# Performance work log

Measured on AMD Instinct MI355X. Metric: run time of the kernel, lower is better.

Reference implementation:

```python
import jax, jax.numpy as jnp
import numpy as np

N_NODES = 100000
N_EDGES = 1600000
D = 128


def setup_inputs() -> dict:
    key = jax.random.key(0)
    k1, k2, k3 = jax.random.split(key, 3)
    x = jax.random.normal(k1, (N_NODES, D), dtype=jnp.float32)
    edge_index = jax.random.randint(k2, (2, N_EDGES), 0, N_NODES, dtype=jnp.int64)
    weight = jax.random.normal(k3, (D, D), dtype=jnp.float32) * (1.0 / np.sqrt(D))
    bias = jnp.zeros((D,), dtype=jnp.float32)
    return {"x": x, "edge_index": edge_index, "weight": weight, "bias": bias}


def reference(x, edge_index, weight, bias):
    # Eval-mode forward: dropout(p=0.5, training=False) is identity.
    N = x.shape[0]
    row, col = edge_index[0], edge_index[1]  # source -> target

    # gcn_norm: add self loops (weight 1), symmetric normalization
    loop = jnp.arange(N, dtype=edge_index.dtype)
    full_row = jnp.concatenate([row, loop])
    full_col = jnp.concatenate([col, loop])
    ew = jnp.ones(full_row.shape[0], dtype=x.dtype)
    deg = jax.ops.segment_sum(ew, full_col, num_segments=N)
    deg_inv_sqrt = jnp.where(deg > 0, jax.lax.rsqrt(jnp.maximum(deg, 1e-12)), 0.0)
    norm = deg_inv_sqrt[full_row] * ew * deg_inv_sqrt[full_col]  # [E+N]

    # linear transform then gather-scale-scatter aggregation
    h = x @ weight.T  # [N, D]
    msgs = h[full_row] * norm[:, None]  # [E+N, D]
    out = jax.ops.segment_sum(msgs, full_col, num_segments=N)
    out = out + bias
    return jax.nn.relu(out)
```

## Files before the change

kernel.cpp:

```cpp
#include <hip/hip_runtime.h>

#define N_NODES 100000
#define N_EDGES 1600000
#define D 128
#define N_STRIPS (N_NODES / 32)

#define BSH   9
#define NBKT  196
#define P_BLK 512
#define EPB   (N_EDGES / P_BLK)
#define ARENA 9216

typedef __bf16 bf16x4 __attribute__((ext_vector_type(4)));
typedef __bf16 bf16x8 __attribute__((ext_vector_type(8)));
typedef float  f32x4  __attribute__((ext_vector_type(4)));

__device__ __forceinline__ void acc8(float (&a)[8], uint4 v) {
    a[0] += __uint_as_float(v.x << 16);
    a[1] += __uint_as_float(v.x & 0xFFFF0000u);
    a[2] += __uint_as_float(v.y << 16);
    a[3] += __uint_as_float(v.y & 0xFFFF0000u);
    a[4] += __uint_as_float(v.z << 16);
    a[5] += __uint_as_float(v.z & 0xFFFF0000u);
    a[6] += __uint_as_float(v.w << 16);
    a[7] += __uint_as_float(v.w & 0xFFFF0000u);
}

__device__ __forceinline__ void gather_node(const int* __restrict__ srcs,
                                            int s, int n,
                                            const unsigned char* hbase,
                                            size_t boff, int lane, int q,
                                            float (&acc)[8]) {
    for (int base = 0; base < n; base += 64) {
        int m = n - base; if (m > 64) m = 64;
        int src_l = (lane < m) ? srcs[s + base + lane] : 0;
        int i = 0;
        for (; i + 4 <= m; i += 4) {
            int sj = __shfl(src_l, i + q);
            uint4 v = *(const uint4*)(hbase + ((size_t)sj + boff));
            acc8(acc, v);
        }
        if (i < m) {
            int sj = __shfl(src_l, i + q);
            if (q < m - i) {
                uint4 v = *(const uint4*)(hbase + ((size_t)sj + boff));
                acc8(acc, v);
            }
        }
    }
}

__global__ __launch_bounds__(1024) void k_scatter(const int* __restrict__ row,
                                                  const int* __restrict__ col,
                                                  const float4* __restrict__ w4,
                                                  int* __restrict__ gcnt,
                                                  unsigned* __restrict__ grec,
                                                  bf16x4* __restrict__ wb4) {
    int b = blockIdx.x, t = threadIdx.x;
    if (b == P_BLK) {
        for (int i = t; i < (D * D) / 4; i += 1024) {
            float4 u = w4[i];
            bf16x4 p;
            p[0] = (__bf16)u.x; p[1] = (__bf16)u.y;
            p[2] = (__bf16)u.z; p[3] = (__bf16)u.w;
            wb4[i] = p;
        }
        return;
    }
    __shared__ int      rec[EPB];
    __shared__ unsigned short kb[EPB];
    __shared__ int      srt[EPB];
    __shared__ int      dofp[EPB];
    __shared__ int      lh[256];
    __shared__ int      sc[256];
    __shared__ int      cur[256];
    __shared__ int      dofk[256];
    if (t < 256) lh[t] = 0;
    __syncthreads();
    int e0 = b * EPB;
    for (int i = t; i < EPB; i += 1024) {
        int r = row[e0 + i], c = col[e0 + i];
        int k = c >> BSH;
        rec[i] = (r << BSH) | (c & ((1 << BSH) - 1));
        kb[i]  = (unsigned short)k;
        atomicAdd(&lh[k], 1);
    }
    __syncthreads();
    int v = 0;
    if (t < 256) { v = lh[t]; sc[t] = v; }
    __syncthreads();
    for (int off = 1; off < 256; off <<= 1) {
        int u = 0;
        if (t < 256 && t >= off) u = sc[t - off];
        __syncthreads();
        if (t < 256) sc[t] += u;
        __syncthreads();
    }
    if (t < 256) {
        int excl = sc[t] - v;
        sc[t]  = excl;
        cur[t] = 0;
        int base = (t < NBKT && v > 0) ? atomicAdd(&gcnt[t], v) : 0;
        dofk[t] = t * ARENA + base - excl;
    }
    __syncthreads();
    for (int i = t; i < EPB; i += 1024) {
        int k = kb[i];
        int p = sc[k] + atomicAdd(&cur[k], 1);
        srt[p]  = rec[i];
        dofp[p] = dofk[k];
    }
    __syncthreads();
    for (int i = t; i < EPB; i += 1024) {
        unsigned dst = (unsigned)(i + dofp[i]);
        if (dst < (unsigned)(NBKT * ARENA))
            grec[dst] = (unsigned)srt[i];
    }
}

__global__ __launch_bounds__(1024) void k_fine(unsigned* __restrict__ grec,
                                               const int* __restrict__ gcnt,
                                               int* __restrict__ deg,
                                               float* __restrict__ dis,
                                               int* __restrict__ start) {
    __shared__ unsigned cache[ARENA];
    __shared__ int fh[512];
    __shared__ int fsc[512];
    int b = blockIdx.x;
    int tid = threadIdx.x;
    int cnt = gcnt[b]; if (cnt > ARENA) cnt = ARENA;
    int gs = b * ARENA;
    if (tid < 512) fh[tid] = 0;
    __syncthreads();
    for (int i = tid; i < cnt; i += 1024) {
        unsigned r = grec[gs + i];
        cache[i] = r;
        atomicAdd(&fh[r & 511], 1);
    }
    __syncthreads();
    int v = 0;
    if (tid < 512) { v = fh[tid]; fsc[tid] = v; }
    __syncthreads();
    for (int off = 1; off < 512; off <<= 1) {
        int u = 0;
        if (tid < 512 && tid >= off) u = fsc[tid - off];
        __syncthreads();
        if (tid < 512) fsc[tid] += u;
        __syncthreads();
    }
    if (tid < 512) {
        int excl = fsc[tid] - v;
        int node = (b << BSH) + tid;
        if (node < N_NODES) {
            deg[node]   = v;
            dis[node]   = rsqrtf((float)v + 1.0f);
            start[node] = gs + excl;
        }
        fh[tid] = excl;
    }
    __syncthreads();
    for (int i = tid; i < cnt; i += 1024) {
        unsigned r = cache[i];
        int pos = atomicAdd(&fh[r & 511], 1);
        grec[gs + pos] = (r >> BSH) << 8;
    }
}

__global__ __launch_bounds__(256) void k_hx(const float* __restrict__ x,
                                            const __bf16* __restrict__ wb,
                                            const float* __restrict__ dis,
                                            __bf16* __restrict__ hb) {
    int wave = threadIdx.x >> 6;
    int lane = threadIdx.x & 63;
    int strip = blockIdx.x * 4 + wave;
    if (strip >= N_STRIPS) return;
    int m0 = strip * 32;
    int l15 = lane & 15;
    int kq  = lane >> 4;

    bf16x8 a[2][4];
    #pragma unroll
    for (int mt = 0; mt < 2; ++mt) {
        const float* ap = x + (size_t)(m0 + mt * 16 + l15) * D + kq * 8;
        #pragma unroll
        for (int ks = 0; ks < 4; ++ks) {
            float4 lo = *(const float4*)(ap + ks * 32);
            float4 hi = *(const float4*)(ap + ks * 32 + 4);
            bf16x8 t;
            t[0] = (__bf16)lo.x; t[1] = (__bf16)lo.y;
            t[2] = (__bf16)lo.z; t[3] = (__bf16)lo.w;
            t[4] = (__bf16)hi.x; t[5] = (__bf16)hi.y;
            t[6] = (__bf16)hi.z; t[7] = (__bf16)hi.w;
            a[mt][ks] = t;
        }
    }

    f32x4 acc[2][8] = {};
    #pragma unroll
    for (int ks = 0; ks < 4; ++ks) {
        #pragma unroll
        for (int nt = 0; nt < 8; ++nt) {
            bf16x8 b = *(const bf16x8*)(wb + (size_t)(nt * 16 + l15) * D + ks * 32 + kq * 8);
            acc[0][nt] = __builtin_amdgcn_mfma_f32_16x16x32_bf16(a[0][ks], b, acc[0][nt], 0, 0, 0);
            acc[1][nt] = __builtin_amdgcn_mfma_f32_16x16x32_bf16(a[1][ks], b, acc[1][nt], 0, 0, 0);
        }
    }

    float dsv[2][4];
    #pragma unroll
    for (int mt = 0; mt < 2; ++mt)
        #pragma unroll
        for (int r = 0; r < 4; ++r)
            dsv[mt][r] = dis[m0 + mt * 16 + kq * 4 + r];

    #pragma unroll
    for (int nt = 0; nt < 8; ++nt) {
        int colj = nt * 16 + l15;
        #pragma unroll
        for (int mt = 0; mt < 2; ++mt) {
            #pragma unroll
            for (int r = 0; r < 4; ++r) {
                int rowi = m0 + mt * 16 + kq * 4 + r;
                hb[(size_t)rowi * D + colj] = (__bf16)(acc[mt][nt][r] * dsv[mt][r]);
            }
        }
    }
}

__global__ __launch_bounds__(256) void k_aggregate(const int* __restrict__ srcs,
                                                   const int* __restrict__ start,
                                                   const int* __restrict__ deg,
                                                   const __bf16* __restrict__ hb,
                                                   const float* __restrict__ dis,
                                                   const float* __restrict__ bias,
                                                   float* __restrict__ out) {
    int wid = (blockIdx.x * 256 + threadIdx.x) >> 6;
    int nodeA = wid * 2;
    if (nodeA >= N_NODES) return;
    int nodeB = nodeA + 1;
    int lane = threadIdx.x & 63;
    int li = lane & 15;
    int q  = lane >> 4;
    const unsigned char* hbase = (const unsigned char*)hb;
    size_t boff = (size_t)li * 16;

    int sA = start[nodeA], nA = deg[nodeA];
    int sB = start[nodeB], nB = deg[nodeB];
    float dA = dis[nodeA], dB = dis[nodeB];

    uint4 selfA = *(const uint4*)(hbase + ((size_t)nodeA * 256 + boff));
    uint4 selfB = *(const uint4*)(hbase + ((size_t)nodeB * 256 + boff));

    float accA[8] = {0.f, 0.f, 0.f, 0.f, 0.f, 0.f, 0.f, 0.f};
    float accB[8] = {0.f, 0.f, 0.f, 0.f, 0.f, 0.f, 0.f, 0.f};

    if (nA <= 64 && nB <= 64) {
        int srcA = (lane < nA) ? srcs[sA + lane] : 0;
        int srcB = (lane < nB) ? srcs[sB + lane] : 0;
        int nmax = nA > nB ? nA : nB;
        #pragma unroll
        for (int i = 0; i < 64; i += 16) {
            if (i >= nmax) break;
            int svA[4], svB[4];
            #pragma unroll
            for (int j = 0; j < 4; ++j) {
                svA[j] = __shfl(srcA, i + 4 * j + q);
                svB[j] = __shfl(srcB, i + 4 * j + q);
            }
            uint4 avA[4], avB[4];
            if (i < nA) {
                #pragma unroll
                for (int j = 0; j < 4; ++j)
                    avA[j] = *(const uint4*)(hbase + ((size_t)svA[j] + boff));
            }
            if (i < nB) {
                #pragma unroll
                for (int j = 0; j < 4; ++j)
                    avB[j] = *(const uint4*)(hbase + ((size_t)svB[j] + boff));
            }
            if (i < nA) {
                #pragma unroll
                for (int j = 0; j < 4; ++j)
                    if (i + 4 * j + q < nA) acc8(accA, avA[j]);
            }
            if (i < nB) {
                #pragma unroll
                for (int j = 0; j < 4; ++j)
                    if (i + 4 * j + q < nB) acc8(accB, avB[j]);
            }
        }
    } else {
        gather_node(srcs, sA, nA, hbase, boff, lane, q, accA);
        gather_node(srcs, sB, nB, hbase, boff, lane, q, accB);
    }

    #pragma unroll
    for (int k = 0; k < 8; ++k) {
        accA[k] += __shfl_xor(accA[k], 16);
        accA[k] += __shfl_xor(accA[k], 32);
        accB[k] += __shfl_xor(accB[k], 16);
        accB[k] += __shfl_xor(accB[k], 32);
    }

    if (q == 0) {
        acc8(accA, selfA);
        acc8(accB, selfB);

        float4 b0 = *(const float4*)(bias + li * 8);
        float4 b1 = *(const float4*)(bias + li * 8 + 4);
        float4 r0, r1;
        r0.x = fmaxf(accA[0] * dA + b0.x, 0.f);
        r0.y = fmaxf(accA[1] * dA + b0.y, 0.f);
        r0.z = fmaxf(accA[2] * dA + b0.z, 0.f);
        r0.w = fmaxf(accA[3] * dA + b0.w, 0.f);
        r1.x = fmaxf(accA[4] * dA + b1.x, 0.f);
        r1.y = fmaxf(accA[5] * dA + b1.y, 0.f);
        r1.z = fmaxf(accA[6] * dA + b1.z, 0.f);
        r1.w = fmaxf(accA[7] * dA + b1.w, 0.f);
        *(float4*)(out + (size_t)nodeA * D + li * 8)     = r0;
        *(float4*)(out + (size_t)nodeA * D + li * 8 + 4) = r1;

        r0.x = fmaxf(accB[0] * dB + b0.x, 0.f);
        r0.y = fmaxf(accB[1] * dB + b0.y, 0.f);
        r0.z = fmaxf(accB[2] * dB + b0.z, 0.f);
        r0.w = fmaxf(accB[3] * dB + b0.w, 0.f);
        r1.x = fmaxf(accB[4] * dB + b1.x, 0.f);
        r1.y = fmaxf(accB[5] * dB + b1.y, 0.f);
        r1.z = fmaxf(accB[6] * dB + b1.z, 0.f);
        r1.w = fmaxf(accB[7] * dB + b1.w, 0.f);
        *(float4*)(out + (size_t)nodeB * D + li * 8)     = r0;
        *(float4*)(out + (size_t)nodeB * D + li * 8 + 4) = r1;
    }
}

extern "C" void kernel_launch(void* const* d_in, const int* in_sizes, int n_in,
                              void* d_out, int out_size, void* d_ws, size_t ws_size,
                              hipStream_t stream) {
    const float* x    = (const float*)d_in[0];
    const int*   ei   = (const int*)d_in[1];
    const float* w    = (const float*)d_in[2];
    const float* bias = (const float*)d_in[3];
    float* out = (float*)d_out;

    char* ws = (char*)d_ws;
    int*      deg    = (int*)ws;              ws += N_NODES * 4;
    float*    dis    = (float*)ws;            ws += N_NODES * 4;
    int*      start  = (int*)ws;              ws += N_NODES * 4;
    int*      gcnt   = (int*)ws;              ws += 256 * 4;
    __bf16*   wb     = (__bf16*)ws;           ws += D * D * 2;
    unsigned* arena  = (unsigned*)ws;         ws += (size_t)NBKT * ARENA * 4;
    __bf16*   hb     = (__bf16*)ws;

    const int* row = ei;
    const int* col = ei + N_EDGES;

    hipMemsetAsync(gcnt, 0, 256 * 4, stream);
    k_scatter  <<<P_BLK + 1, 1024, 0, stream>>>(row, col, (const float4*)w, gcnt, arena, (bf16x4*)wb);
    k_fine     <<<NBKT, 1024, 0, stream>>>(arena, gcnt, deg, dis, start);
    k_hx       <<<(N_STRIPS + 3) / 4, 256, 0, stream>>>(x, wb, dis, hb);
    k_aggregate<<<(N_NODES / 2 * 64) / 256, 256, 0, stream>>>((const int*)arena, start, deg, hb, dis, bias, out);
}
```

Baseline: 222.7 us.

## Fuse coarse scatter and fine bucket sort into one kernel with grid barrier

Merges the coarse partition kernel and the per-bucket fine sort into a single persistent kernel. A global atomic counter acts as a grid-wide barrier, and the shared-memory arena is reused between the two phases. Partition blocks are halved to 256 so that all blocks can be co-resident and the barrier cannot deadlock, with the weight bf16 conversion moved to block NBKT after the barrier. This removes one kernel launch and its drain gap, at the cost of a spin barrier, fewer and larger partition blocks, and a reliance on every block being resident at once.

```diff
diff --git a/kernel.cpp b/kernel.cpp
--- a/kernel.cpp
+++ b/kernel.cpp
@@ -7,7 +7,7 @@
 
 #define BSH   9
 #define NBKT  196
-#define P_BLK 512
+#define P_BLK 256
 #define EPB   (N_EDGES / P_BLK)
 #define ARENA 9216
 
@@ -50,14 +50,121 @@
     }
 }
 
-__global__ __launch_bounds__(1024) void k_scatter(const int* __restrict__ row,
-                                                  const int* __restrict__ col,
-                                                  const float4* __restrict__ w4,
-                                                  int* __restrict__ gcnt,
-                                                  unsigned* __restrict__ grec,
-                                                  bf16x4* __restrict__ wb4) {
+__global__ __launch_bounds__(1024) void k_part(const int* __restrict__ row,
+                                               const int* __restrict__ col,
+                                               const float4* __restrict__ w4,
+                                               int* __restrict__ gcnt,
+                                               unsigned* __restrict__ arena,
+                                               bf16x4* __restrict__ wb4,
+                                               int* __restrict__ deg,
+                                               float* __restrict__ dis,
+                                               int* __restrict__ start) {
+    __shared__ unsigned smem[23040];
     int b = blockIdx.x, t = threadIdx.x;
-    if (b == P_BLK) {
+    int* done = gcnt + 256;
+
+    {
+        int*            rec  = (int*)smem;
+        unsigned short* kb   = (unsigned short*)(smem + 6272);
+        int*            srt  = (int*)(smem + 9408);
+        int*            dofp = (int*)(smem + 15680);
+        int*            lh   = (int*)(smem + 21952);
+        int*            sc   = lh + 256;
+        int*            cur  = sc + 256;
+        int*            dofk = cur + 256;
+
+        if (t < 256) lh[t] = 0;
+        __syncthreads();
+        int e0 = b * EPB;
+        for (int i = t; i < EPB; i += 1024) {
+            int r = row[e0 + i], c = col[e0 + i];
+            int k = c >> BSH;
+            rec[i] = (r << BSH) | (c & ((1 << BSH) - 1));
+            kb[i]  = (unsigned short)k;
+            atomicAdd(&lh[k], 1);
+        }
+        __syncthreads();
+        int v = 0;
+        if (t < 256) { v = lh[t]; sc[t] = v; }
+        __syncthreads();
+        for (int off = 1; off < 256; off <<= 1) {
+            int u = 0;
+            if (t < 256 && t >= off) u = sc[t - off];
+            __syncthreads();
+            if (t < 256) sc[t] += u;
+            __syncthreads();
+        }
+        if (t < 256) {
+            int excl = sc[t] - v;
+            sc[t]  = excl;
+            cur[t] = 0;
+            int base = (t < NBKT && v > 0) ? atomicAdd(&gcnt[t], v) : 0;
+            dofk[t] = t * ARENA + base - excl;
+        }
+        __syncthreads();
+        for (int i = t; i < EPB; i += 1024) {
+            int k = kb[i];
+            int p = sc[k] + atomicAdd(&cur[k], 1);
+            srt[p]  = rec[i];
+            dofp[p] = dofk[k];
+        }
+        __syncthreads();
+        for (int i = t; i < EPB; i += 1024) {
+            unsigned dst = (unsigned)(i + dofp[i]);
+            if (dst < (unsigned)(NBKT * ARENA))
+                arena[dst] = (unsigned)srt[i];
+        }
+    }
+
+    __syncthreads();
+    if (t == 0) {
+        __threadfence();
+        __hip_atomic_fetch_add(done, 1, __ATOMIC_ACQ_REL, __HIP_MEMORY_SCOPE_AGENT);
+        while (__hip_atomic_load(done, __ATOMIC_ACQUIRE, __HIP_MEMORY_SCOPE_AGENT) < P_BLK) {}
+    }
+    __syncthreads();
+
+    if (b < NBKT) {
+        unsigned* cache = smem;
+        int*      fh    = (int*)(smem + 9216);
+        int*      fsc   = (int*)(smem + 9728);
+        int cnt = gcnt[b]; if (cnt > ARENA) cnt = ARENA;
+        int gs = b * ARENA;
+        if (t < 512) fh[t] = 0;
+        __syncthreads();
+        for (int i = t; i < cnt; i += 1024) {
+            unsigned r = arena[gs + i];
+            cache[i] = r;
+            atomicAdd(&fh[r & 511], 1);
+        }
+        __syncthreads();
+        int v = 0;
+        if (t < 512) { v = fh[t]; fsc[t] = v; }
+        __syncthreads();
+        for (int off = 1; off < 512; off <<= 1) {
+            int u = 0;
+            if (t < 512 && t >= off) u = fsc[t - off];
+            __syncthreads();
+            if (t < 512) fsc[t] += u;
+            __syncthreads();
+        }
+        if (t < 512) {
+            int excl = fsc[t] - v;
+            int node = (b << BSH) + t;
+            if (node < N_NODES) {
+                deg[node]   = v;
+                dis[node]   = rsqrtf((float)v + 1.0f);
+                start[node] = gs + excl;
+            }
+            fh[t] = excl;
+        }
+        __syncthreads();
+        for (int i = t; i < cnt; i += 1024) {
+            unsigned r = cache[i];
+            int pos = atomicAdd(&fh[r & 511], 1);
+            arena[gs + pos] = (r >> BSH) << 8;
+        }
+    } else if (b == NBKT) {
         for (int i = t; i < (D * D) / 4; i += 1024) {
             float4 u = w4[i];
             bf16x4 p;
@@ -65,104 +172,6 @@
             p[2] = (__bf16)u.z; p[3] = (__bf16)u.w;
             wb4[i] = p;
         }
-        return;
-    }
-    __shared__ int      rec[EPB];
-    __shared__ unsigned short kb[EPB];
-    __shared__ int      srt[EPB];
-    __shared__ int      dofp[EPB];
-    __shared__ int      lh[256];
-    __shared__ int      sc[256];
-    __shared__ int      cur[256];
-    __shared__ int      dofk[256];
-    if (t < 256) lh[t] = 0;
-    __syncthreads();
-    int e0 = b * EPB;
-    for (int i = t; i < EPB; i += 1024) {
-        int r = row[e0 + i], c = col[e0 + i];
-        int k = c >> BSH;
-        rec[i] = (r << BSH) | (c & ((1 << BSH) - 1));
-        kb[i]  = (unsigned short)k;
-        atomicAdd(&lh[k], 1);
-    }
-    __syncthreads();
-    int v = 0;
-    if (t < 256) { v = lh[t]; sc[t] = v; }
-    __syncthreads();
-    for (int off = 1; off < 256; off <<= 1) {
-        int u = 0;
-        if (t < 256 && t >= off) u = sc[t - off];
-        __syncthreads();
-        if (t < 256) sc[t] += u;
-        __syncthreads();
-    }
-    if (t < 256) {
-        int excl = sc[t] - v;
-        sc[t]  = excl;
-        cur[t] = 0;
-        int base = (t < NBKT && v > 0) ? atomicAdd(&gcnt[t], v) : 0;
-        dofk[t] = t * ARENA + base - excl;
-    }
-    __syncthreads();
-    for (int i = t; i < EPB; i += 1024) {
-        int k = kb[i];
-        int p = sc[k] + atomicAdd(&cur[k], 1);
-        srt[p]  = rec[i];
-        dofp[p] = dofk[k];
-    }
-    __syncthreads();
-    for (int i = t; i < EPB; i += 1024) {
-        unsigned dst = (unsigned)(i + dofp[i]);
-        if (dst < (unsigned)(NBKT * ARENA))
-            grec[dst] = (unsigned)srt[i];
-    }
-}
-
-__global__ __launch_bounds__(1024) void k_fine(unsigned* __restrict__ grec,
-                                               const int* __restrict__ gcnt,
-                                               int* __restrict__ deg,
-                                               float* __restrict__ dis,
-                                               int* __restrict__ start) {
-    __shared__ unsigned cache[ARENA];
-    __shared__ int fh[512];
-    __shared__ int fsc[512];
-    int b = blockIdx.x;
-    int tid = threadIdx.x;
-    int cnt = gcnt[b]; if (cnt > ARENA) cnt = ARENA;
-    int gs = b * ARENA;
-    if (tid < 512) fh[tid] = 0;
-    __syncthreads();
-    for (int i = tid; i < cnt; i += 1024) {
-        unsigned r = grec[gs + i];
-        cache[i] = r;
-        atomicAdd(&fh[r & 511], 1);
-    }
-    __syncthreads();
-    int v = 0;
-    if (tid < 512) { v = fh[tid]; fsc[tid] = v; }
-    __syncthreads();
-    for (int off = 1; off < 512; off <<= 1) {
-        int u = 0;
-        if (tid < 512 && tid >= off) u = fsc[tid - off];
-        __syncthreads();
-        if (tid < 512) fsc[tid] += u;
-        __syncthreads();
-    }
-    if (tid < 512) {
-        int excl = fsc[tid] - v;
-        int node = (b << BSH) + tid;
-        if (node < N_NODES) {
-            deg[node]   = v;
-            dis[node]   = rsqrtf((float)v + 1.0f);
-            start[node] = gs + excl;
-        }
-        fh[tid] = excl;
-    }
-    __syncthreads();
-    for (int i = tid; i < cnt; i += 1024) {
-        unsigned r = cache[i];
-        int pos = atomicAdd(&fh[r & 511], 1);
-        grec[gs + pos] = (r >> BSH) << 8;
     }
 }
 
@@ -346,7 +355,7 @@
     int*      deg    = (int*)ws;              ws += N_NODES * 4;
     float*    dis    = (float*)ws;            ws += N_NODES * 4;
     int*      start  = (int*)ws;              ws += N_NODES * 4;
-    int*      gcnt   = (int*)ws;              ws += 256 * 4;
+    int*      gcnt   = (int*)ws;              ws += 512 * 4;
     __bf16*   wb     = (__bf16*)ws;           ws += D * D * 2;
     unsigned* arena  = (unsigned*)ws;         ws += (size_t)NBKT * ARENA * 4;
     __bf16*   hb     = (__bf16*)ws;
@@ -354,9 +363,9 @@
     const int* row = ei;
     const int* col = ei + N_EDGES;
 
-    hipMemsetAsync(gcnt, 0, 256 * 4, stream);
-    k_scatter  <<<P_BLK + 1, 1024, 0, stream>>>(row, col, (const float4*)w, gcnt, arena, (bf16x4*)wb);
-    k_fine     <<<NBKT, 1024, 0, stream>>>(arena, gcnt, deg, dis, start);
+    hipMemsetAsync(gcnt, 0, 512 * 4, stream);
+    k_part     <<<P_BLK, 1024, 0, stream>>>(row, col, (const float4*)w, gcnt, arena,
+                                            (bf16x4*)wb, deg, dis, start);
     k_hx       <<<(N_STRIPS + 3) / 4, 256, 0, stream>>>(x, wb, dis, hb);
     k_aggregate<<<(N_NODES / 2 * 64) / 256, 256, 0, stream>>>((const int*)arena, start, deg, hb, dis, bias, out);
 }
```

After: 246.4 us. 1.11x slower.
